# Optimization experiments

Measured on AMD Instinct MI355X. Metric: run time of the kernel, lower is better.

Reference implementation:

```python
import jax, jax.numpy as jnp
import numpy as np

N, DEG, F, H, OUT = 50000, 16, 128, 128, 64


def _lstm_aggr(neigh, w_ih, w_hh, b_ih, b_hh):
    # neigh: [N, D, F] fixed-degree neighbor features; run LSTM over D steps,
    # return final hidden state [N, H] (PyG SAGEConv 'lstm' aggregation).
    n, d, f = neigh.shape
    h_dim = w_hh.shape[1]

    def step(carry, xt):
        h, c = carry
        gates = xt @ w_ih.T + b_ih + h @ w_hh.T + b_hh  # [N, 4H]
        i, fg, g, o = jnp.split(gates, 4, axis=-1)      # torch gate order i,f,g,o
        i = jax.nn.sigmoid(i)
        fg = jax.nn.sigmoid(fg)
        g = jnp.tanh(g)
        o = jax.nn.sigmoid(o)
        c = fg * c + i * g
        h = o * jnp.tanh(c)
        return (h, c), None

    h0 = jnp.zeros((n, h_dim), neigh.dtype)
    (h, _), _ = jax.lax.scan(step, (h0, h0), jnp.swapaxes(neigh, 0, 1))
    return h


def _sage_lstm(x, src, w_ih, w_hh, b_ih, b_hh, wl, bl, wr):
    # SAGEConv: out = lin_l(lstm_aggr(x[neighbors])) + lin_r(x)
    neigh = x[src]                                   # [N, D, F] gather
    aggr = _lstm_aggr(neigh, w_ih, w_hh, b_ih, b_hh)  # [N, H]
    return aggr @ wl.T + bl + x @ wr.T


def setup_inputs() -> dict:
    key = jax.random.key(0)
    ks = jax.random.split(key, 16)
    x = jax.random.normal(ks[0], (N, F), dtype=jnp.float32)
    # fixed-degree graph: dst = arange(N) each repeated DEG times (sorted, as
    # PyG lstm aggregation requires), src random -> edge_index [2, N*DEG]
    src = jax.random.randint(ks[1], (N * DEG,), 0, N, dtype=jnp.int64)
    dst = jnp.repeat(jnp.arange(N, dtype=jnp.int64), DEG)
    edge_index = jnp.stack([src, dst])
    s = 1.0 / np.sqrt(H)
    def u(k, shape):
        return jax.random.uniform(k, shape, jnp.float32, -s, s)
    params = {
        # layer 1 (input F -> hidden H)
        "w_ih1": u(ks[2], (4 * H, F)), "w_hh1": u(ks[3], (4 * H, H)),
        "b_ih1": u(ks[4], (4 * H,)), "b_hh1": u(ks[5], (4 * H,)),
        "lin_l1_w": u(ks[6], (H, H)), "lin_l1_b": u(ks[6], (H,)),
        "lin_r1_w": u(ks[7], (H, F)),
        # layer 2 (H -> H)
        "w_ih2": u(ks[8], (4 * H, H)), "w_hh2": u(ks[9], (4 * H, H)),
        "b_ih2": u(ks[10], (4 * H,)), "b_hh2": u(ks[11], (4 * H,)),
        "lin_l2_w": u(ks[12], (H, H)), "lin_l2_b": u(ks[12], (H,)),
        "lin_r2_w": u(ks[13], (H, H)),
        # output head
        "lin_w": u(ks[14], (OUT, H)), "lin_b": u(ks[15], (OUT,)),
    }
    return {"x": x, "edge_index": edge_index, **params}


def reference(x, edge_index,
              w_ih1, w_hh1, b_ih1, b_hh1, lin_l1_w, lin_l1_b, lin_r1_w,
              w_ih2, w_hh2, b_ih2, b_hh2, lin_l2_w, lin_l2_b, lin_r2_w,
              lin_w, lin_b):
    n = x.shape[0]
    deg = edge_index.shape[1] // n
    src = edge_index[0].reshape(n, deg)  # fixed-degree neighbor matrix
    h = _sage_lstm(x, src, w_ih1, w_hh1, b_ih1, b_hh1, lin_l1_w, lin_l1_b, lin_r1_w)
    h = jax.nn.relu(h)
    h = _sage_lstm(h, src, w_ih2, w_hh2, b_ih2, b_hh2, lin_l2_w, lin_l2_b, lin_r2_w)
    h = jax.nn.relu(h)
    return h @ lin_w.T + lin_b
```

## Files before the change

kernel.cpp:

```cpp
#include <hip/hip_runtime.h>
#include <stdint.h>

#define NN 50000
#define DEG 16
#define MT 32
#define NBLK ((NN + MT - 1) / MT)
#define LOG2E 1.4426950408889634f

typedef short bf16x8 __attribute__((ext_vector_type(8)));
typedef float f32x4 __attribute__((ext_vector_type(4)));
typedef unsigned short u16;
typedef unsigned int u32;

static __device__ __forceinline__ u16 f2bf(float f) {
  union { float f; u32 u; } v; v.f = f;
  u32 u = v.u + 0x7FFFu + ((v.u >> 16) & 1u);
  return (u16)(u >> 16);
}
static __device__ __forceinline__ float rcp_(float x) {
  return __builtin_amdgcn_rcpf(x);
}
static __device__ __forceinline__ float ex2_(float x) {
  return __builtin_amdgcn_exp2f(x);
}
static __device__ __forceinline__ void gload_lds16(const void* g, void* l) {
  __builtin_amdgcn_global_load_lds(
      (const __attribute__((address_space(1))) void*)g,
      (__attribute__((address_space(3))) void*)l, 16, 0, 0);
}

__global__ void k_prep(const float* __restrict__ x, u16* __restrict__ xb,
                       const float* __restrict__ wih1, const float* __restrict__ whh1, u16* __restrict__ wpk1,
                       const float* __restrict__ wih2, const float* __restrict__ whh2, u16* __restrict__ wpk2,
                       const float* __restrict__ lr1, const float* __restrict__ ll1, u16* __restrict__ epk1,
                       const float* __restrict__ lr2, const float* __restrict__ ll2, u16* __restrict__ epk2,
                       const float* __restrict__ linw, u16* __restrict__ hpk,
                       const float* __restrict__ bi1, const float* __restrict__ bh1, float* __restrict__ bs1,
                       const float* __restrict__ bi2, const float* __restrict__ bh2, float* __restrict__ bs2) {
  int b = blockIdx.x;
  if (b < 128) {
    const float* wih = (b < 64) ? wih1 : wih2;
    const float* whh = (b < 64) ? whh1 : whh2;
    u16* wpk = (b < 64) ? wpk1 : wpk2;
    int t = (b & 63) * 256 + threadIdx.x;
    int lane = t & 63, kt = (t >> 6) & 7, g = (t >> 9) & 3, w = (t >> 11) & 7;
    int col = g * 128 + w * 16 + (lane & 15);
    int k0 = kt * 32 + (lane >> 4) * 8;
    float sc = (g == 2) ? 2.f * LOG2E : LOG2E;
#pragma unroll
    for (int j = 0; j < 8; ++j) {
      int k = k0 + j;
      float v = (k < 128) ? wih[col * 128 + k] : whh[col * 128 + k - 128];
      wpk[t * 8 + j] = f2bf(sc * v);
    }
  } else if (b < 160) {
    const float* lrw = (b < 144) ? lr1 : lr2;
    const float* llw = (b < 144) ? ll1 : ll2;
    u16* epk = (b < 144) ? epk1 : epk2;
    int t = ((b - 128) & 15) * 256 + threadIdx.x;
    int lane = t & 63, kt = (t >> 6) & 7, w = (t >> 9) & 7;
    int col = w * 16 + (lane & 15);
    int k0 = kt * 32 + (lane >> 4) * 8;
#pragma unroll
    for (int j = 0; j < 8; ++j) {
      int k = k0 + j;
      epk[t * 8 + j] = f2bf(k < 128 ? lrw[col * 128 + k] : llw[col * 128 + k - 128]);
    }
  } else if (b < 164) {
    int t = (b - 160) * 256 + threadIdx.x;
    int lane = t & 63, kt = (t >> 6) & 3, w = (t >> 8) & 3;
    int col = w * 16 + (lane & 15);
    int k0 = kt * 32 + (lane >> 4) * 8;
#pragma unroll
    for (int j = 0; j < 8; ++j) hpk[t * 8 + j] = f2bf(linw[col * 128 + k0 + j]);
  } else if (b < 168) {
    int t = (b - 164) * 256 + threadIdx.x;
    if (t < 1024) {
      int i = t & 511;
      float sc = ((i >> 7) == 2) ? 2.f * LOG2E : LOG2E;
      if (t < 512) bs1[i] = sc * (bi1[i] + bh1[i]);
      else bs2[i] = sc * (bi2[i] + bh2[i]);
    }
  } else {
    int i = (b - 168) * 256 + threadIdx.x;
    int stride = (gridDim.x - 168) * 256;
    for (; i < NN * 128 / 4; i += stride) {
      float4 v = ((const float4*)x)[i];
      ushort4 o;
      o.x = f2bf(v.x); o.y = f2bf(v.y); o.z = f2bf(v.z); o.w = f2bf(v.w);
      ((ushort4*)xb)[i] = o;
    }
  }
}

template <int L2>
__global__ __launch_bounds__(512, 2) void k_layer(
    const u16* __restrict__ xin, const int* __restrict__ src,
    const u16* __restrict__ wpk, const float* __restrict__ bsum,
    const u16* __restrict__ epk, const float* __restrict__ linlb,
    u16* __restrict__ hout, const u16* __restrict__ hpk,
    const float* __restrict__ linb, float* __restrict__ dout) {
  __shared__ __align__(16) u16 AX[2][MT * 128];
  __shared__ __align__(16) u16 AH[2][MT * 128];
  __shared__ int IDX[MT * DEG];

  const int tid = threadIdx.x;
  const int w = tid >> 6, l = tid & 63;
  const int lr = l & 15, lh = l >> 4;
  const int node0 = blockIdx.x * MT;

  bf16x8 wreg[4][8];
#pragma unroll
  for (int g = 0; g < 4; ++g)
#pragma unroll
    for (int kt = 0; kt < 8; ++kt)
      wreg[g][kt] = *(const bf16x8*)(wpk + (size_t)(((w * 4 + g) * 8 + kt) * 64 + l) * 8);

  IDX[tid] = (node0 + (tid >> 4) < NN) ? src[node0 * DEG + tid] : 0;

  float gb[4];
#pragma unroll
  for (int g = 0; g < 4; ++g) gb[g] = bsum[g * 128 + w * 16 + lr];
  float eb = linlb[w * 16 + lr];
  __syncthreads();

  const int grow = w * 4 + lh;
  {
    int idx = IDX[grow * DEG];
    const char* gsw = (const char*)(xin + (size_t)idx * 128) +
                      ((lr * 16) ^ ((grow & 15) << 4));
    gload_lds16(gsw, &AX[0][(w * 4) * 128]);
  }

  f32x4 c[2];
  c[0] = (f32x4){0.f, 0.f, 0.f, 0.f};
  c[1] = (f32x4){0.f, 0.f, 0.f, 0.f};
  __syncthreads();

#pragma unroll 1
  for (int step = 0; step < DEG; ++step) {
    const int cb = step & 1, nb = cb ^ 1;
    const u16* axc = AX[cb];
    const u16* ahc = AH[cb];

    {
      int idx = (step < DEG - 1) ? IDX[grow * DEG + step + 1]
                                 : ((node0 + grow < NN) ? node0 + grow : NN - 1);
      const char* gsw = (const char*)(xin + (size_t)idx * 128) +
                        ((lr * 16) ^ ((grow & 15) << 4));
      gload_lds16(gsw, &AX[nb][(w * 4) * 128]);
    }

    f32x4 acc[2][4];
#pragma unroll
    for (int mt = 0; mt < 2; ++mt)
#pragma unroll
      for (int g = 0; g < 4; ++g)
        acc[mt][g] = (f32x4){gb[g], gb[g], gb[g], gb[g]};

#pragma unroll
    for (int kt = 0; kt < 4; ++kt) {
      bf16x8 af[2];
#pragma unroll
      for (int mt = 0; mt < 2; ++mt) {
        int row = mt * 16 + lr;
        af[mt] = *(const bf16x8*)((const char*)axc + row * 256 +
                                  ((kt * 64 + lh * 16) ^ ((row & 15) << 4)));
      }
#pragma unroll
      for (int g = 0; g < 4; ++g)
#pragma unroll
        for (int mt = 0; mt < 2; ++mt)
          acc[mt][g] = __builtin_amdgcn_mfma_f32_16x16x32_bf16(af[mt], wreg[g][kt], acc[mt][g], 0, 0, 0);
    }

    if (step) {
#pragma unroll
      for (int kt = 0; kt < 4; ++kt) {
        bf16x8 af[2];
#pragma unroll
        for (int mt = 0; mt < 2; ++mt) {
          int row = mt * 16 + lr;
          af[mt] = *(const bf16x8*)((const char*)ahc + row * 256 +
                                    ((kt * 64 + lh * 16) ^ ((row & 15) << 4)));
        }
#pragma unroll
        for (int g = 0; g < 4; ++g)
#pragma unroll
          for (int mt = 0; mt < 2; ++mt)
            acc[mt][g] = __builtin_amdgcn_mfma_f32_16x16x32_bf16(af[mt], wreg[g][4 + kt], acc[mt][g], 0, 0, 0);
      }
    }

#pragma unroll
    for (int mt = 0; mt < 2; ++mt)
#pragma unroll
      for (int r = 0; r < 4; ++r) {
        float iv = rcp_(1.f + ex2_(-acc[mt][0][r]));
        float fv = rcp_(1.f + ex2_(-acc[mt][1][r]));
        float gv = 1.f - 2.f * rcp_(1.f + ex2_(acc[mt][2][r]));
        float ov = rcp_(1.f + ex2_(-acc[mt][3][r]));
        float cv = fv * c[mt][r] + iv * gv;
        c[mt][r] = cv;
        float th = 1.f - 2.f * rcp_(1.f + ex2_(2.f * LOG2E * cv));
        int row = mt * 16 + lh * 4 + r;
        int jj = 2 * (w * 16 + lr);
        *(u16*)((char*)AH[nb] + row * 256 + (jj ^ ((row & 15) << 4))) =
            f2bf(ov * th);
      }
    __syncthreads();
  }

  f32x4 eacc[2];
  eacc[0] = (f32x4){eb, eb, eb, eb};
  eacc[1] = (f32x4){eb, eb, eb, eb};
#pragma unroll
  for (int kt = 0; kt < 8; ++kt) {
    const u16* srcb = (kt < 4) ? AX[0] : AH[0];
    int kb = (kt & 3) * 64 + lh * 16;
    bf16x8 af[2];
#pragma unroll
    for (int mt = 0; mt < 2; ++mt) {
      int row = mt * 16 + lr;
      af[mt] = *(const bf16x8*)((const char*)srcb + row * 256 +
                                (kb ^ ((row & 15) << 4)));
    }
    bf16x8 bf = *(const bf16x8*)(epk + (size_t)((w * 8 + kt) * 64 + l) * 8);
#pragma unroll
    for (int mt = 0; mt < 2; ++mt)
      eacc[mt] = __builtin_amdgcn_mfma_f32_16x16x32_bf16(af[mt], bf, eacc[mt], 0, 0, 0);
  }

  if constexpr (!L2) {
#pragma unroll
    for (int mt = 0; mt < 2; ++mt)
#pragma unroll
      for (int r = 0; r < 4; ++r) {
        int node = node0 + mt * 16 + lh * 4 + r;
        if (node < NN) {
          float v = fmaxf(eacc[mt][r], 0.f);
          hout[(size_t)node * 128 + w * 16 + lr] = f2bf(v);
        }
      }
  } else {
#pragma unroll
    for (int mt = 0; mt < 2; ++mt)
#pragma unroll
      for (int r = 0; r < 4; ++r) {
        int row = mt * 16 + lh * 4 + r;
        float v = fmaxf(eacc[mt][r], 0.f);
        int jj = 2 * (w * 16 + lr);
        *(u16*)((char*)AX[1] + row * 256 + (jj ^ ((row & 15) << 4))) = f2bf(v);
      }
    __syncthreads();
    if (w < 4) {
      float hb = linb[w * 16 + lr];
      f32x4 hacc[2];
      hacc[0] = (f32x4){hb, hb, hb, hb};
      hacc[1] = (f32x4){hb, hb, hb, hb};
#pragma unroll
      for (int kt = 0; kt < 4; ++kt) {
        bf16x8 af[2];
#pragma unroll
        for (int mt = 0; mt < 2; ++mt) {
          int row = mt * 16 + lr;
          af[mt] = *(const bf16x8*)((const char*)AX[1] + row * 256 +
                                    ((kt * 64 + lh * 16) ^ ((row & 15) << 4)));
        }
        bf16x8 bf = *(const bf16x8*)(hpk + (size_t)((w * 4 + kt) * 64 + l) * 8);
#pragma unroll
        for (int mt = 0; mt < 2; ++mt)
          hacc[mt] = __builtin_amdgcn_mfma_f32_16x16x32_bf16(af[mt], bf, hacc[mt], 0, 0, 0);
      }
#pragma unroll
      for (int mt = 0; mt < 2; ++mt)
#pragma unroll
        for (int r = 0; r < 4; ++r) {
          int node = node0 + mt * 16 + lh * 4 + r;
          if (node < NN) dout[(size_t)node * 64 + w * 16 + lr] = hacc[mt][r];
        }
    }
  }
}

extern "C" void kernel_launch(void* const* d_in, const int* in_sizes, int n_in,
                              void* d_out, int out_size, void* d_ws, size_t ws_size,
                              hipStream_t stream) {
  const float* x    = (const float*)d_in[0];
  const int*   edge = (const int*)d_in[1];
  const float* wih1 = (const float*)d_in[2];
  const float* whh1 = (const float*)d_in[3];
  const float* bih1 = (const float*)d_in[4];
  const float* bhh1 = (const float*)d_in[5];
  const float* ll1w = (const float*)d_in[6];
  const float* ll1b = (const float*)d_in[7];
  const float* lr1w = (const float*)d_in[8];
  const float* wih2 = (const float*)d_in[9];
  const float* whh2 = (const float*)d_in[10];
  const float* bih2 = (const float*)d_in[11];
  const float* bhh2 = (const float*)d_in[12];
  const float* ll2w = (const float*)d_in[13];
  const float* ll2b = (const float*)d_in[14];
  const float* lr2w = (const float*)d_in[15];
  const float* linw = (const float*)d_in[16];
  const float* linb = (const float*)d_in[17];

  char* ws = (char*)d_ws;
  u16* xb    = (u16*)(ws);
  u16* h1b   = (u16*)(ws + 12800000);
  u16* wpk1  = (u16*)(ws + 25600000);
  u16* wpk2  = (u16*)(ws + 25862144);
  u16* epk1  = (u16*)(ws + 26124288);
  u16* epk2  = (u16*)(ws + 26189824);
  u16* hpk   = (u16*)(ws + 26255360);
  float* bs1 = (float*)(ws + 26271744);
  float* bs2 = (float*)(ws + 26273792);

  k_prep<<<1000, 256, 0, stream>>>(x, xb,
                                   wih1, whh1, wpk1, wih2, whh2, wpk2,
                                   lr1w, ll1w, epk1, lr2w, ll2w, epk2,
                                   linw, hpk,
                                   bih1, bhh1, bs1, bih2, bhh2, bs2);
  k_layer<0><<<NBLK, 512, 0, stream>>>(xb, edge, wpk1, bs1, epk1, ll1b,
                                       h1b, nullptr, nullptr, nullptr);
  k_layer<1><<<NBLK, 512, 0, stream>>>(h1b, edge, wpk2, bs2, epk2, ll2b,
                                       nullptr, hpk, linb, (float*)d_out);
}
```

Before: 583.9 us.

## Software-pipeline LSTM steps: overlap next x-projection MFMAs with current gate math

Restructures the 16-step LSTM recurrence into a two-step unrolled pipeline with a triple-buffered neighbor-feature LDS ring. The input projection for step t+1 is issued alongside the elementwise gate math of step t, so its MFMAs can overlap the transcendental work and the recurrent critical path shrinks to the h-part only. This costs an extra 8 KB of LDS, a second accumulator set of 32 floats that raises register pressure, and buffer rotation that must leave the self-node features in AX[1] for the epilogue.

```diff
diff --git a/kernel.cpp b/kernel.cpp
--- a/kernel.cpp
+++ b/kernel.cpp
@@ -93,6 +93,66 @@
   }
 }
 
+
+#define GATHER(DCODE, PDST)                                                   \
+  do {                                                                        \
+    int idx_;                                                                 \
+    if ((DCODE) < DEG) idx_ = IDX[grow * DEG + (DCODE)];                      \
+    else idx_ = (node0 + grow < NN) ? node0 + grow : NN - 1;                  \
+    const char* gsw_ = (const char*)(xin + (size_t)idx_ * 128) +              \
+                       ((lr * 16) ^ ((grow & 15) << 4));                      \
+    gload_lds16(gsw_, (PDST) + (w * 4) * 128);                                \
+  } while (0)
+
+#define GATE_XPART(ACC, PSRC)                                                 \
+  do {                                                                        \
+    _Pragma("unroll") for (int mt = 0; mt < 2; ++mt)                          \
+        _Pragma("unroll") for (int g = 0; g < 4; ++g)                         \
+            ACC[mt][g] = (f32x4){gb[g], gb[g], gb[g], gb[g]};                 \
+    _Pragma("unroll") for (int kt = 0; kt < 4; ++kt) {                        \
+      bf16x8 af0 = *(const bf16x8*)((const char*)(PSRC) + lr * 256 +          \
+                                    ((kt * 64 + lh * 16) ^ ((lr & 15) << 4))); \
+      bf16x8 af1 = *(const bf16x8*)((const char*)(PSRC) + (16 + lr) * 256 +   \
+                                    ((kt * 64 + lh * 16) ^ ((lr & 15) << 4))); \
+      _Pragma("unroll") for (int g = 0; g < 4; ++g) {                         \
+        ACC[0][g] = __builtin_amdgcn_mfma_f32_16x16x32_bf16(af0, wreg[g][kt], ACC[0][g], 0, 0, 0); \
+        ACC[1][g] = __builtin_amdgcn_mfma_f32_16x16x32_bf16(af1, wreg[g][kt], ACC[1][g], 0, 0, 0); \
+      }                                                                       \
+    }                                                                         \
+  } while (0)
+
+#define GATE_HPART(ACC, PSRC)                                                 \
+  do {                                                                        \
+    _Pragma("unroll") for (int kt = 0; kt < 4; ++kt) {                        \
+      bf16x8 af0 = *(const bf16x8*)((const char*)(PSRC) + lr * 256 +          \
+                                    ((kt * 64 + lh * 16) ^ ((lr & 15) << 4))); \
+      bf16x8 af1 = *(const bf16x8*)((const char*)(PSRC) + (16 + lr) * 256 +   \
+                                    ((kt * 64 + lh * 16) ^ ((lr & 15) << 4))); \
+      _Pragma("unroll") for (int g = 0; g < 4; ++g) {                         \
+        ACC[0][g] = __builtin_amdgcn_mfma_f32_16x16x32_bf16(af0, wreg[g][4 + kt], ACC[0][g], 0, 0, 0); \
+        ACC[1][g] = __builtin_amdgcn_mfma_f32_16x16x32_bf16(af1, wreg[g][4 + kt], ACC[1][g], 0, 0, 0); \
+      }                                                                       \
+    }                                                                         \
+  } while (0)
+
+#define GATE_EW(ACC, AHDST)                                                   \
+  do {                                                                        \
+    _Pragma("unroll") for (int mt = 0; mt < 2; ++mt)                          \
+        _Pragma("unroll") for (int r = 0; r < 4; ++r) {                       \
+      float iv = rcp_(1.f + ex2_(-ACC[mt][0][r]));                            \
+      float fv = rcp_(1.f + ex2_(-ACC[mt][1][r]));                            \
+      float gv = 1.f - 2.f * rcp_(1.f + ex2_(ACC[mt][2][r]));                 \
+      float ov = rcp_(1.f + ex2_(-ACC[mt][3][r]));                            \
+      float cv = fv * c[mt][r] + iv * gv;                                     \
+      c[mt][r] = cv;                                                          \
+      float th = 1.f - 2.f * rcp_(1.f + ex2_(2.f * LOG2E * cv));              \
+      int row = mt * 16 + lh * 4 + r;                                         \
+      int jj = 2 * (w * 16 + lr);                                             \
+      *(u16*)((char*)(AHDST) + row * 256 + (jj ^ ((row & 15) << 4))) =        \
+          f2bf(ov * th);                                                      \
+    }                                                                         \
+  } while (0)
+
 template <int L2>
 __global__ __launch_bounds__(512, 2) void k_layer(
     const u16* __restrict__ xin, const int* __restrict__ src,
@@ -100,7 +160,7 @@
     const u16* __restrict__ epk, const float* __restrict__ linlb,
     u16* __restrict__ hout, const u16* __restrict__ hpk,
     const float* __restrict__ linb, float* __restrict__ dout) {
-  __shared__ __align__(16) u16 AX[2][MT * 128];
+  __shared__ __align__(16) u16 AX[3][MT * 128];
   __shared__ __align__(16) u16 AH[2][MT * 128];
   __shared__ int IDX[MT * DEG];
 
@@ -108,6 +168,7 @@
   const int w = tid >> 6, l = tid & 63;
   const int lr = l & 15, lh = l >> 4;
   const int node0 = blockIdx.x * MT;
+  const int grow = w * 4 + lh;
 
   bf16x8 wreg[4][8];
 #pragma unroll
@@ -121,102 +182,45 @@
   float gb[4];
 #pragma unroll
   for (int g = 0; g < 4; ++g) gb[g] = bsum[g * 128 + w * 16 + lr];
-  float eb = linlb[w * 16 + lr];
   __syncthreads();
 
-  const int grow = w * 4 + lh;
-  {
-    int idx = IDX[grow * DEG];
-    const char* gsw = (const char*)(xin + (size_t)idx * 128) +
-                      ((lr * 16) ^ ((grow & 15) << 4));
-    gload_lds16(gsw, &AX[0][(w * 4) * 128]);
-  }
+  GATHER(0, AX[0]);
+  GATHER(1, AX[1]);
 
   f32x4 c[2];
   c[0] = (f32x4){0.f, 0.f, 0.f, 0.f};
   c[1] = (f32x4){0.f, 0.f, 0.f, 0.f};
   __syncthreads();
 
+  f32x4 accE[2][4], accO[2][4];
+  GATE_XPART(accE, AX[0]);
+
+  u16 *p0 = AX[0], *p1 = AX[1], *p2 = AX[2];
+
 #pragma unroll 1
-  for (int step = 0; step < DEG; ++step) {
-    const int cb = step & 1, nb = cb ^ 1;
-    const u16* axc = AX[cb];
-    const u16* ahc = AH[cb];
-
-    {
-      int idx = (step < DEG - 1) ? IDX[grow * DEG + step + 1]
-                                 : ((node0 + grow < NN) ? node0 + grow : NN - 1);
-      const char* gsw = (const char*)(xin + (size_t)idx * 128) +
-                        ((lr * 16) ^ ((grow & 15) << 4));
-      gload_lds16(gsw, &AX[nb][(w * 4) * 128]);
-    }
-
-    f32x4 acc[2][4];
-#pragma unroll
-    for (int mt = 0; mt < 2; ++mt)
-#pragma unroll
-      for (int g = 0; g < 4; ++g)
-        acc[mt][g] = (f32x4){gb[g], gb[g], gb[g], gb[g]};
-
-#pragma unroll
-    for (int kt = 0; kt < 4; ++kt) {
-      bf16x8 af[2];
-#pragma unroll
-      for (int mt = 0; mt < 2; ++mt) {
-        int row = mt * 16 + lr;
-        af[mt] = *(const bf16x8*)((const char*)axc + row * 256 +
-                                  ((kt * 64 + lh * 16) ^ ((row & 15) << 4)));
-      }
-#pragma unroll
-      for (int g = 0; g < 4; ++g)
-#pragma unroll
-        for (int mt = 0; mt < 2; ++mt)
-          acc[mt][g] = __builtin_amdgcn_mfma_f32_16x16x32_bf16(af[mt], wreg[g][kt], acc[mt][g], 0, 0, 0);
-    }
-
-    if (step) {
-#pragma unroll
-      for (int kt = 0; kt < 4; ++kt) {
-        bf16x8 af[2];
-#pragma unroll
-        for (int mt = 0; mt < 2; ++mt) {
-          int row = mt * 16 + lr;
-          af[mt] = *(const bf16x8*)((const char*)ahc + row * 256 +
-                                    ((kt * 64 + lh * 16) ^ ((row & 15) << 4)));
-        }
-#pragma unroll
-        for (int g = 0; g < 4; ++g)
-#pragma unroll
-          for (int mt = 0; mt < 2; ++mt)
-            acc[mt][g] = __builtin_amdgcn_mfma_f32_16x16x32_bf16(af[mt], wreg[g][4 + kt], acc[mt][g], 0, 0, 0);
-      }
-    }
-
-#pragma unroll
-    for (int mt = 0; mt < 2; ++mt)
-#pragma unroll
-      for (int r = 0; r < 4; ++r) {
-        float iv = rcp_(1.f + ex2_(-acc[mt][0][r]));
-        float fv = rcp_(1.f + ex2_(-acc[mt][1][r]));
-        float gv = 1.f - 2.f * rcp_(1.f + ex2_(acc[mt][2][r]));
-        float ov = rcp_(1.f + ex2_(-acc[mt][3][r]));
-        float cv = fv * c[mt][r] + iv * gv;
-        c[mt][r] = cv;
-        float th = 1.f - 2.f * rcp_(1.f + ex2_(2.f * LOG2E * cv));
-        int row = mt * 16 + lh * 4 + r;
-        int jj = 2 * (w * 16 + lr);
-        *(u16*)((char*)AH[nb] + row * 256 + (jj ^ ((row & 15) << 4))) =
-            f2bf(ov * th);
-      }
+  for (int it = 0; it < 8; ++it) {
+    GATHER(2 * it + 2, p2);
+    if (it) GATE_HPART(accE, AH[0]);
+    GATE_XPART(accO, p1);
+    GATE_EW(accE, AH[1]);
     __syncthreads();
+    { u16* t_ = p0; p0 = p1; p1 = p2; p2 = t_; }
+
+    if (it < 7) GATHER(2 * it + 3, p2);
+    GATE_HPART(accO, AH[1]);
+    if (it < 7) GATE_XPART(accE, p1);
+    GATE_EW(accO, AH[0]);
+    __syncthreads();
+    { u16* t_ = p0; p0 = p1; p1 = p2; p2 = t_; }
   }
 
+  float eb = linlb[w * 16 + lr];
   f32x4 eacc[2];
   eacc[0] = (f32x4){eb, eb, eb, eb};
   eacc[1] = (f32x4){eb, eb, eb, eb};
 #pragma unroll
   for (int kt = 0; kt < 8; ++kt) {
-    const u16* srcb = (kt < 4) ? AX[0] : AH[0];
+    const u16* srcb = (kt < 4) ? AX[1] : AH[0];
     int kb = (kt & 3) * 64 + lh * 16;
     bf16x8 af[2];
 #pragma unroll
@@ -250,7 +254,7 @@
         int row = mt * 16 + lh * 4 + r;
         float v = fmaxf(eacc[mt][r], 0.f);
         int jj = 2 * (w * 16 + lr);
-        *(u16*)((char*)AX[1] + row * 256 + (jj ^ ((row & 15) << 4))) = f2bf(v);
+        *(u16*)((char*)AX[0] + row * 256 + (jj ^ ((row & 15) << 4))) = f2bf(v);
       }
     __syncthreads();
     if (w < 4) {
@@ -264,7 +268,7 @@
 #pragma unroll
         for (int mt = 0; mt < 2; ++mt) {
           int row = mt * 16 + lr;
-          af[mt] = *(const bf16x8*)((const char*)AX[1] + row * 256 +
+          af[mt] = *(const bf16x8*)((const char*)AX[0] + row * 256 +
                                     ((kt * 64 + lh * 16) ^ ((row & 15) << 4)));
         }
         bf16x8 bf = *(const bf16x8*)(hpk + (size_t)((w * 4 + kt) * 64 + l) * 8);
```

Measured after the change: 591.7 us. About the same (+1.3%).

## Triple-buffer neighbor gathers and use partial vmcnt waits to prefetch two steps ahead

Applied to the files above, without the earlier changes.

The single double-buffered X tile becomes a three-deep ring, so neighbor rows for step+2 are gathered while step runs. Each full __syncthreads is replaced by an explicit s_waitcnt vmcnt(1) plus s_barrier, which leaves one gather in flight across the barrier. The goal is to hide the latency of the random-row global gather behind the recurrent MFMA work. It costs an extra 8 KB of LDS per block, which could affect the 2-blocks-per-CU occupancy, and the layer-2 head scratch moves to AH[1].

```diff
diff --git a/kernel.cpp b/kernel.cpp
--- a/kernel.cpp
+++ b/kernel.cpp
@@ -93,6 +93,24 @@
   }
 }
 
+
+#define GATHER(DCODE, PDST)                                                   \
+  do {                                                                        \
+    int idx_;                                                                 \
+    if ((DCODE) < DEG) idx_ = IDX[grow * DEG + (DCODE)];                      \
+    else idx_ = (node0 + grow < NN) ? node0 + grow : NN - 1;                  \
+    const char* gsw_ = (const char*)(xin + (size_t)idx_ * 128) +              \
+                       ((lr * 16) ^ ((grow & 15) << 4));                      \
+    gload_lds16(gsw_, (PDST) + (w * 4) * 128);                                \
+  } while (0)
+
+#define CBAR(N)                                                               \
+  do {                                                                        \
+    asm volatile("s_waitcnt vmcnt(" #N ") lgkmcnt(0)" ::: "memory");          \
+    __builtin_amdgcn_s_barrier();                                             \
+    __builtin_amdgcn_sched_barrier(0);                                        \
+  } while (0)
+
 template <int L2>
 __global__ __launch_bounds__(512, 2) void k_layer(
     const u16* __restrict__ xin, const int* __restrict__ src,
@@ -100,7 +118,7 @@
     const u16* __restrict__ epk, const float* __restrict__ linlb,
     u16* __restrict__ hout, const u16* __restrict__ hpk,
     const float* __restrict__ linb, float* __restrict__ dout) {
-  __shared__ __align__(16) u16 AX[2][MT * 128];
+  __shared__ __align__(16) u16 AX[3][MT * 128];
   __shared__ __align__(16) u16 AH[2][MT * 128];
   __shared__ int IDX[MT * DEG];
 
@@ -108,6 +126,7 @@
   const int w = tid >> 6, l = tid & 63;
   const int lr = l & 15, lh = l >> 4;
   const int node0 = blockIdx.x * MT;
+  const int grow = w * 4 + lh;
 
   bf16x8 wreg[4][8];
 #pragma unroll
@@ -124,32 +143,21 @@
   float eb = linlb[w * 16 + lr];
   __syncthreads();
 
-  const int grow = w * 4 + lh;
-  {
-    int idx = IDX[grow * DEG];
-    const char* gsw = (const char*)(xin + (size_t)idx * 128) +
-                      ((lr * 16) ^ ((grow & 15) << 4));
-    gload_lds16(gsw, &AX[0][(w * 4) * 128]);
-  }
+  GATHER(0, AX[0]);
+  GATHER(1, AX[1]);
 
   f32x4 c[2];
   c[0] = (f32x4){0.f, 0.f, 0.f, 0.f};
   c[1] = (f32x4){0.f, 0.f, 0.f, 0.f};
-  __syncthreads();
+  CBAR(1);
+
+  u16 *pA = AX[0], *pB = AX[1], *pC = AX[2];
 
 #pragma unroll 1
   for (int step = 0; step < DEG; ++step) {
     const int cb = step & 1, nb = cb ^ 1;
-    const u16* axc = AX[cb];
-    const u16* ahc = AH[cb];
-
-    {
-      int idx = (step < DEG - 1) ? IDX[grow * DEG + step + 1]
-                                 : ((node0 + grow < NN) ? node0 + grow : NN - 1);
-      const char* gsw = (const char*)(xin + (size_t)idx * 128) +
-                        ((lr * 16) ^ ((grow & 15) << 4));
-      gload_lds16(gsw, &AX[nb][(w * 4) * 128]);
-    }
+
+    if (step < DEG - 1) GATHER(step + 2, pC);
 
     f32x4 acc[2][4];
 #pragma unroll
@@ -164,7 +172,7 @@
 #pragma unroll
       for (int mt = 0; mt < 2; ++mt) {
         int row = mt * 16 + lr;
-        af[mt] = *(const bf16x8*)((const char*)axc + row * 256 +
+        af[mt] = *(const bf16x8*)((const char*)pA + row * 256 +
                                   ((kt * 64 + lh * 16) ^ ((row & 15) << 4)));
       }
 #pragma unroll
@@ -181,7 +189,7 @@
 #pragma unroll
         for (int mt = 0; mt < 2; ++mt) {
           int row = mt * 16 + lr;
-          af[mt] = *(const bf16x8*)((const char*)ahc + row * 256 +
+          af[mt] = *(const bf16x8*)((const char*)AH[cb] + row * 256 +
                                     ((kt * 64 + lh * 16) ^ ((row & 15) << 4)));
         }
 #pragma unroll
@@ -208,7 +216,12 @@
         *(u16*)((char*)AH[nb] + row * 256 + (jj ^ ((row & 15) << 4))) =
             f2bf(ov * th);
       }
-    __syncthreads();
+
+    if (step < DEG - 1) CBAR(1);
+    else CBAR(0);
+
+    u16* t_ = pA; pA = pB; pB = t_; 
+    t_ = pB; pB = pC; pC = t_;
   }
 
   f32x4 eacc[2];
@@ -216,7 +229,7 @@
   eacc[1] = (f32x4){eb, eb, eb, eb};
 #pragma unroll
   for (int kt = 0; kt < 8; ++kt) {
-    const u16* srcb = (kt < 4) ? AX[0] : AH[0];
+    const u16* srcb = (kt < 4) ? pA : AH[0];
     int kb = (kt & 3) * 64 + lh * 16;
     bf16x8 af[2];
 #pragma unroll
@@ -250,7 +263,7 @@
         int row = mt * 16 + lh * 4 + r;
         float v = fmaxf(eacc[mt][r], 0.f);
         int jj = 2 * (w * 16 + lr);
-        *(u16*)((char*)AX[1] + row * 256 + (jj ^ ((row & 15) << 4))) = f2bf(v);
+        *(u16*)((char*)AH[1] + row * 256 + (jj ^ ((row & 15) << 4))) = f2bf(v);
       }
     __syncthreads();
     if (w < 4) {
@@ -264,7 +277,7 @@
 #pragma unroll
         for (int mt = 0; mt < 2; ++mt) {
           int row = mt * 16 + lr;
-          af[mt] = *(const bf16x8*)((const char*)AX[1] + row * 256 +
+          af[mt] = *(const bf16x8*)((const char*)AH[1] + row * 256 +
                                     ((kt * 64 + lh * 16) ^ ((row & 15) << 4)));
         }
         bf16x8 bf = *(const bf16x8*)(hpk + (size_t)((w * 4 + kt) * 64 + l) * 8);
```

Measured after the change: 530.0 us. -9.2%, faster.
